# Kernel tuning notes

Measured on AMD Instinct MI355X. Metric: run time of the kernel, lower is better.

## Reference

```python
import jax, jax.numpy as jnp
import numpy as np

NEG_SLOPE = 0.2  # PyG GATConv default negative_slope


def gat_conv(x, src, dst, n_nodes, W, a_src, a_dst, b, concat):
    # x: [N, F_in], W: [F_in, H*C], a_src/a_dst: [H, C], b: [H*C] or [C]
    H, C = a_src.shape
    h = (x @ W).reshape(n_nodes, H, C)              # [N, H, C]
    e_s = jnp.sum(h * a_src, axis=-1)               # [N, H]
    e_d = jnp.sum(h * a_dst, axis=-1)               # [N, H]
    e = jax.nn.leaky_relu(e_s[src] + e_d[dst], NEG_SLOPE)  # [E, H]
    # segment softmax over incoming edges of each destination node
    m = jax.ops.segment_max(e, dst, num_segments=n_nodes)
    m = jnp.where(jnp.isfinite(m), m, 0.0)
    p = jnp.exp(e - m[dst])                         # [E, H]
    s = jax.ops.segment_sum(p, dst, num_segments=n_nodes)
    alpha = p / (s[dst] + 1e-16)                    # [E, H]
    out = jax.ops.segment_sum(h[src] * alpha[:, :, None], dst, num_segments=n_nodes)  # [N, H, C]
    out = out.reshape(n_nodes, H * C) if concat else out.mean(axis=1)
    return out + b


def setup_inputs() -> dict:
    key = jax.random.key(0)
    ks = jax.random.split(key, 20)
    N, E = 50000, 800000
    F_in, C, H = 128, 64, 4
    sc = 0.05
    inp = {
        "x": jax.random.normal(ks[0], (N, F_in), dtype=jnp.float32),
        "edge_index": jax.random.randint(ks[1], (2, E), 0, N, dtype=jnp.int64),
        # conv1: F_in -> C x H heads, concat
        "W1": jax.random.normal(ks[2], (F_in, H * C), dtype=jnp.float32) * sc,
        "a1_src": jax.random.normal(ks[3], (H, C), dtype=jnp.float32) * sc,
        "a1_dst": jax.random.normal(ks[4], (H, C), dtype=jnp.float32) * sc,
        "b1": jnp.zeros((H * C,), dtype=jnp.float32),
        # conv2: H*C -> C x H heads, concat
        "W2": jax.random.normal(ks[5], (H * C, H * C), dtype=jnp.float32) * sc,
        "a2_src": jax.random.normal(ks[6], (H, C), dtype=jnp.float32) * sc,
        "a2_dst": jax.random.normal(ks[7], (H, C), dtype=jnp.float32) * sc,
        "b2": jnp.zeros((H * C,), dtype=jnp.float32),
        # conv3: H*C -> C, 1 head, concat=False (mean)
        "W3": jax.random.normal(ks[8], (H * C, C), dtype=jnp.float32) * sc,
        "a3_src": jax.random.normal(ks[9], (1, C), dtype=jnp.float32) * sc,
        "a3_dst": jax.random.normal(ks[10], (1, C), dtype=jnp.float32) * sc,
        "b3": jnp.zeros((C,), dtype=jnp.float32),
        # node classification head: C -> 2
        "cls_W": jax.random.normal(ks[11], (C, 2), dtype=jnp.float32) * sc,
        "cls_b": jnp.zeros((2,), dtype=jnp.float32),
    }
    return inp


def reference(x, edge_index, W1, a1_src, a1_dst, b1, W2, a2_src, a2_dst, b2,
              W3, a3_src, a3_dst, b3, cls_W, cls_b):
    N = x.shape[0]
    # PyG GATConv default: add self loops
    loop = jnp.arange(N, dtype=edge_index.dtype)
    ei = jnp.concatenate([edge_index, jnp.stack([loop, loop])], axis=1)
    src, dst = ei[0], ei[1]

    h = jax.nn.elu(gat_conv(x, src, dst, N, W1, a1_src, a1_dst, b1, concat=True))
    h = jax.nn.elu(gat_conv(h, src, dst, N, W2, a2_src, a2_dst, b2, concat=True))
    h = gat_conv(h, src, dst, N, W3, a3_src, a3_dst, b3, concat=False)  # [N, C]

    node_output = h @ cls_W + cls_b  # [N, 2]
    link_embedding = h               # [N, C]
    return node_output, link_embedding
```

## Files before the change

### kernel.cpp

```cpp
#include <hip/hip_runtime.h>
#include <math.h>


typedef unsigned short ushort;
typedef __attribute__((ext_vector_type(8))) short bf16x8;
typedef __attribute__((ext_vector_type(4))) float f32x4;

#define LOG2E 1.4426950408889634f

static __device__ __forceinline__ ushort f2bf(float f) {
    unsigned x = __float_as_uint(f);
    unsigned r = (x + 0x7FFF + ((x >> 16) & 1)) >> 16;
    return (ushort)r;
}
static __device__ __forceinline__ float bf2f(ushort u) {
    return __uint_as_float(((unsigned)u) << 16);
}


__global__ void count_deg(const int* __restrict__ ei, int E, int* __restrict__ deg) {
    int i = blockIdx.x * blockDim.x + threadIdx.x;
    int stride = gridDim.x * blockDim.x;
    for (int e = i; e < E; e += stride) {
        int d = ei[E + e];
        atomicAdd(&deg[d], 1);
    }
}

__global__ void scan_local(const int* __restrict__ deg, int* __restrict__ offsets,
                           int* __restrict__ blockSums, int N) {
    int tid = threadIdx.x;
    int lane = tid & 63;
    int wv = tid >> 6;
    int base = blockIdx.x * 1024 + tid * 4;
    int v[4];
#pragma unroll
    for (int j = 0; j < 4; ++j) {
        int idx = base + j;
        v[j] = (idx < N) ? ((deg[idx] + 1 + 7) & ~7) : 0;
    }
    int tsum = v[0] + v[1] + v[2] + v[3];
    int inc = tsum;
#pragma unroll
    for (int off = 1; off < 64; off <<= 1) {
        int u = __shfl_up(inc, off);
        if (lane >= off) inc += u;
    }
    __shared__ int wtot[4];
    if (lane == 63) wtot[wv] = inc;
    __syncthreads();
    int wbase = 0;
#pragma unroll
    for (int w = 0; w < 4; ++w)
        if (w < wv) wbase += wtot[w];
    int run = wbase + inc - tsum;
#pragma unroll
    for (int j = 0; j < 4; ++j) {
        int idx = base + j;
        if (idx < N) offsets[idx] = run;
        run += v[j];
    }
    if (tid == 255) blockSums[blockIdx.x] = wbase + inc;
}

__global__ void scan_blocks(const int* __restrict__ blockSums, int* __restrict__ blockBase,
                            int* __restrict__ offsets, int N, int nblk) {
    int lane = threadIdx.x & 63;
    int v = (lane < nblk) ? blockSums[lane] : 0;
    int inc = v;
#pragma unroll
    for (int off = 1; off < 64; off <<= 1) {
        int u = __shfl_up(inc, off);
        if (lane >= off) inc += u;
    }
    if (lane < nblk) blockBase[lane] = inc - v;
    if (lane == 63) offsets[N] = inc;
}

__global__ void scan_add(int* __restrict__ offsets, const int* __restrict__ blockBase, int N) {
    int i = blockIdx.x * blockDim.x + threadIdx.x;
    if (i < N) offsets[i] += blockBase[i >> 10];
}

__global__ void fill_sent(int* __restrict__ csr_src, int cap, int N) {
    int i = blockIdx.x * blockDim.x + threadIdx.x;
    if (i < cap) csr_src[i] = N;
}

__global__ void fill_self(const int* __restrict__ offsets, int* __restrict__ counter,
                          int* __restrict__ csr_src, int N) {
    int i = blockIdx.x * blockDim.x + threadIdx.x;
    if (i < N) {
        csr_src[offsets[i]] = i;
        counter[i] = 1;
    }
}

__global__ void fill_edges(const int* __restrict__ ei, int E,
                           const int* __restrict__ offsets, int* __restrict__ counter,
                           int* __restrict__ csr_src) {
    int i = blockIdx.x * blockDim.x + threadIdx.x;
    int stride = gridDim.x * blockDim.x;
    for (int e = i; e < E; e += stride) {
        int s = ei[e];
        int d = ei[E + e];
        int pos = offsets[d] + atomicAdd(&counter[d], 1);
        csr_src[pos] = s;
    }
}


__global__ void xsplit(const float* __restrict__ X, ushort* __restrict__ Xh,
                       ushort* __restrict__ Xl, int total4) {
    int i = blockIdx.x * blockDim.x + threadIdx.x;
    if (i >= total4) return;
    float4 v = *(const float4*)(X + (size_t)i * 4);
    ushort4 h, l;
    h.x = f2bf(v.x); l.x = f2bf(v.x - bf2f(h.x));
    h.y = f2bf(v.y); l.y = f2bf(v.y - bf2f(h.y));
    h.z = f2bf(v.z); l.z = f2bf(v.z - bf2f(h.z));
    h.w = f2bf(v.w); l.w = f2bf(v.w - bf2f(h.w));
    *(ushort4*)(Xh + (size_t)i * 4) = h;
    *(ushort4*)(Xl + (size_t)i * 4) = l;
}

__global__ void wtrans_bf(const float* __restrict__ W, ushort* __restrict__ Wt,
                          int K, int N) {
    int id = blockIdx.x * blockDim.x + threadIdx.x;
    if (id >= K * N) return;
    int k = id % K, n = id / K;
    Wt[id] = f2bf(W[(size_t)k * N + n]);
}


template<int BM, int BN, int WM, int WN, int THREADS>
__global__ __launch_bounds__(THREADS) void gemm_mfma(const ushort* __restrict__ Ah,
                                                     const ushort* __restrict__ Al,
                                                     const ushort* __restrict__ Bh,
                                                     ushort* __restrict__ Cb,
                                                     int M, int N, int K) {
    constexpr int BK = 32, PAD = 8;
    constexpr int MI = BM / WM / 16;
    constexpr int NI = BN / WN / 16;
    static_assert(WM * WN * 64 == THREADS, "wave grid mismatch");
    __shared__ ushort As[2][BM][BK + PAD];
    __shared__ ushort Bs[BN][BK + PAD];

    int tid = threadIdx.x;
    int lane = tid & 63;
    int wid = tid >> 6;
    int fr = lane & 15;
    int fg = lane >> 4;
    int wm0 = (wid / WN) * (BM / WM);
    int wn0 = (wid % WN) * (BN / WN);
    int mBase = blockIdx.x * BM;
    int nBase = blockIdx.y * BN;

    f32x4 acc[MI][NI];
#pragma unroll
    for (int mi = 0; mi < MI; ++mi)
#pragma unroll
        for (int ni = 0; ni < NI; ++ni) acc[mi][ni] = (f32x4)0.0f;

    constexpr int ACH = BM * BK / 8;
    constexpr int BCH = BN * BK / 8;

    const int KI = K / BK;
    for (int t = 0; t < KI; ++t) {
        int k0 = t * BK;
        for (int q = tid; q < ACH; q += THREADS) {
            int row = q >> 2;
            int sl = (q & 3) * 8;
            int gm = mBase + row;
            if (gm >= M) gm = M - 1;
            size_t off = (size_t)gm * K + k0 + sl;
            *(bf16x8*)&As[0][row][sl] = *(const bf16x8*)(Ah + off);
            *(bf16x8*)&As[1][row][sl] = *(const bf16x8*)(Al + off);
        }
        for (int q = tid; q < BCH; q += THREADS) {
            int row = q >> 2;
            int sl = (q & 3) * 8;
            size_t off = (size_t)(nBase + row) * K + k0 + sl;
            *(bf16x8*)&Bs[row][sl] = *(const bf16x8*)(Bh + off);
        }
        __syncthreads();

        bf16x8 afh[MI], afl[MI], bfh[NI];
#pragma unroll
        for (int mi = 0; mi < MI; ++mi) {
            afh[mi] = *(const bf16x8*)&As[0][wm0 + mi * 16 + fr][fg * 8];
            afl[mi] = *(const bf16x8*)&As[1][wm0 + mi * 16 + fr][fg * 8];
        }
#pragma unroll
        for (int ni = 0; ni < NI; ++ni)
            bfh[ni] = *(const bf16x8*)&Bs[wn0 + ni * 16 + fr][fg * 8];
#pragma unroll
        for (int mi = 0; mi < MI; ++mi)
#pragma unroll
            for (int ni = 0; ni < NI; ++ni) {
                acc[mi][ni] = __builtin_amdgcn_mfma_f32_16x16x32_bf16(
                    afh[mi], bfh[ni], acc[mi][ni], 0, 0, 0);
                acc[mi][ni] = __builtin_amdgcn_mfma_f32_16x16x32_bf16(
                    afl[mi], bfh[ni], acc[mi][ni], 0, 0, 0);
            }
        __syncthreads();
    }

#pragma unroll
    for (int mi = 0; mi < MI; ++mi) {
#pragma unroll
        for (int j = 0; j < 4; ++j) {
            int gm = mBase + wm0 + mi * 16 + fg * 4 + j;
            if (gm >= M) continue;
#pragma unroll
            for (int ni = 0; ni < NI; ++ni) {
                int gn = nBase + wn0 + ni * 16 + fr;
                Cb[(size_t)gm * N + gn] = f2bf(acc[mi][ni][j]);
            }
        }
    }
}


template<int HC, int H>
__global__ void attn_coef(ushort* __restrict__ hb,
                          const float* __restrict__ a_src,
                          const float* __restrict__ a_dst,
                          float* __restrict__ e_s, float* __restrict__ e_d, int N) {
    int wid = (int)((blockIdx.x * (size_t)blockDim.x + threadIdx.x) >> 6);
    int lane = threadIdx.x & 63;
    if (wid > N) return;
    if (wid == N) {
        if constexpr (HC == 256) {
            ushort4 z = {0, 0, 0, 0};
            *(ushort4*)(hb + (size_t)N * 256 + lane * 4) = z;
        } else {
            hb[(size_t)N * HC + lane] = 0;
        }
        if (lane < H) e_s[(size_t)N * H + lane] = -1e30f;
        return;
    }
    if constexpr (HC == 256) {
        ushort4 q = *(const ushort4*)(hb + (size_t)wid * 256 + lane * 4);
        float4 as = *(const float4*)(a_src + lane * 4);
        float4 ad = *(const float4*)(a_dst + lane * 4);
        float h0 = bf2f(q.x), h1 = bf2f(q.y), h2 = bf2f(q.z), h3 = bf2f(q.w);
        float ps = h0 * as.x + h1 * as.y + h2 * as.z + h3 * as.w;
        float pd = h0 * ad.x + h1 * ad.y + h2 * ad.z + h3 * ad.w;
#pragma unroll
        for (int off = 1; off <= 8; off <<= 1) {
            ps += __shfl_xor(ps, off);
            pd += __shfl_xor(pd, off);
        }
        if ((lane & 15) == 0) {
            int hd = lane >> 4;
            e_s[(size_t)wid * H + hd] = ps * LOG2E;
            e_d[(size_t)wid * H + hd] = pd * LOG2E;
        }
    } else {
        float hv = bf2f(hb[(size_t)wid * HC + lane]);
        float ps = hv * a_src[lane];
        float pd = hv * a_dst[lane];
#pragma unroll
        for (int off = 1; off <= 32; off <<= 1) {
            ps += __shfl_xor(ps, off);
            pd += __shfl_xor(pd, off);
        }
        if (lane == 0) {
            e_s[wid] = ps * LOG2E;
            e_d[wid] = pd * LOG2E;
        }
    }
}


template<int HC, int H, bool ELU, bool SPLIT>
__global__ void aggregate(const ushort* __restrict__ hb,
                          const float* __restrict__ e_s, const float* __restrict__ e_d,
                          const int* __restrict__ offsets, const int* __restrict__ csr_src,
                          const float* __restrict__ bias,
                          float* __restrict__ out,
                          ushort* __restrict__ oh, ushort* __restrict__ ol, int N) {
    constexpr int U = 8;
    int wid = (int)((blockIdx.x * (size_t)blockDim.x + threadIdx.x) >> 6);
    int lane = threadIdx.x & 63;
    if (wid >= N) return;
    constexpr int VEC = HC / 64;
    constexpr int C = HC / H;
    constexpr int ROWSH = (HC == 256) ? 9 : 7;
    int hd = (lane * VEC) / C;
    float ed = e_d[(size_t)wid * H + hd];
    int beg = offsets[wid], end = offsets[wid + 1];
    const char* hbB = (const char*)hb;
    const char* esB = (const char*)e_s;
    unsigned laneOff = (unsigned)lane * (VEC * 2);

    float s = 0.0f;
    float acc[VEC];
#pragma unroll
    for (int j = 0; j < VEC; ++j) acc[j] = 0.0f;

    for (int k = beg; k < end; k += U) {
        int sidx[U];
#pragma unroll
        for (int u = 0; u < U; ++u) sidx[u] = csr_src[k + u];
        float e[U];
#pragma unroll
        for (int u = 0; u < U; ++u)
            e[u] = *(const float*)(esB + (((unsigned)(sidx[u] * H + hd)) << 2));
        ushort4 hv4[U];
        ushort  hv1[U];
        if constexpr (VEC == 4) {
#pragma unroll
            for (int u = 0; u < U; ++u)
                hv4[u] = *(const ushort4*)(hbB + (((unsigned)sidx[u]) << ROWSH) + laneOff);
        } else {
#pragma unroll
            for (int u = 0; u < U; ++u)
                hv1[u] = *(const ushort*)(hbB + (((unsigned)sidx[u]) << ROWSH) + laneOff);
        }
        float p[U];
        float psum = 0.0f;
#pragma unroll
        for (int u = 0; u < U; ++u) {
            float t = e[u] + ed;
            t = (t >= 0.0f) ? t : 0.2f * t;
            p[u] = __builtin_amdgcn_exp2f(t);
            psum += p[u];
        }
        s += psum;
        if constexpr (VEC == 4) {
#pragma unroll
            for (int u = 0; u < U; ++u) {
                acc[0] += p[u] * bf2f(hv4[u].x);
                acc[1] += p[u] * bf2f(hv4[u].y);
                acc[2] += p[u] * bf2f(hv4[u].z);
                acc[3] += p[u] * bf2f(hv4[u].w);
            }
        } else {
#pragma unroll
            for (int u = 0; u < U; ++u) acc[0] += p[u] * bf2f(hv1[u]);
        }
    }
    float inv = 1.0f / (s + 1e-16f);
    float o[VEC];
#pragma unroll
    for (int j = 0; j < VEC; ++j) {
        int f = lane * VEC + j;
        o[j] = acc[j] * inv + bias[f];
        if constexpr (ELU) o[j] = (o[j] > 0.0f) ? o[j] : expm1f(o[j]);
    }
    if constexpr (SPLIT) {
        if constexpr (VEC == 4) {
            ushort4 h4, l4;
            h4.x = f2bf(o[0]); l4.x = f2bf(o[0] - bf2f(h4.x));
            h4.y = f2bf(o[1]); l4.y = f2bf(o[1] - bf2f(h4.y));
            h4.z = f2bf(o[2]); l4.z = f2bf(o[2] - bf2f(h4.z));
            h4.w = f2bf(o[3]); l4.w = f2bf(o[3] - bf2f(h4.w));
            *(ushort4*)(oh + (size_t)wid * HC + lane * 4) = h4;
            *(ushort4*)(ol + (size_t)wid * HC + lane * 4) = l4;
        } else {
            ushort h1 = f2bf(o[0]);
            oh[(size_t)wid * HC + lane] = h1;
            ol[(size_t)wid * HC + lane] = f2bf(o[0] - bf2f(h1));
        }
    } else {
#pragma unroll
        for (int j = 0; j < VEC; ++j)
            out[(size_t)wid * HC + lane * VEC + j] = o[j];
    }
}


__global__ void cls_head(const float* __restrict__ h3, const float* __restrict__ W,
                         const float* __restrict__ b, float* __restrict__ out, int N) {
    int wid = (int)((blockIdx.x * (size_t)blockDim.x + threadIdx.x) >> 6);
    int lane = threadIdx.x & 63;
    if (wid >= N) return;
    float v = h3[(size_t)wid * 64 + lane];
    float p0 = v * W[lane * 2 + 0];
    float p1 = v * W[lane * 2 + 1];
#pragma unroll
    for (int off = 1; off <= 32; off <<= 1) {
        p0 += __shfl_xor(p0, off);
        p1 += __shfl_xor(p1, off);
    }
    if (lane == 0) {
        out[(size_t)wid * 2 + 0] = p0 + b[0];
        out[(size_t)wid * 2 + 1] = p1 + b[1];
    }
}


extern "C" void kernel_launch(void* const* d_in, const int* in_sizes, int n_in,
                              void* d_out, int out_size, void* d_ws, size_t ws_size,
                              hipStream_t stream) {
    const float* x      = (const float*)d_in[0];
    const int*   ei     = (const int*)d_in[1];
    const float* W1     = (const float*)d_in[2];
    const float* a1_src = (const float*)d_in[3];
    const float* a1_dst = (const float*)d_in[4];
    const float* b1     = (const float*)d_in[5];
    const float* W2     = (const float*)d_in[6];
    const float* a2_src = (const float*)d_in[7];
    const float* a2_dst = (const float*)d_in[8];
    const float* b2     = (const float*)d_in[9];
    const float* W3     = (const float*)d_in[10];
    const float* a3_src = (const float*)d_in[11];
    const float* a3_dst = (const float*)d_in[12];
    const float* b3     = (const float*)d_in[13];
    const float* cls_W  = (const float*)d_in[14];
    const float* cls_b  = (const float*)d_in[15];

    const int N = in_sizes[0] / 128;
    const int E = in_sizes[1] / 2;
    const int ETcap = E + 8 * N + 64;
    const int HC = 256;
    const int nScanBlk = (N + 1023) / 1024;

    char* w = (char*)d_ws;
    auto carve = [&](size_t bytes) {
        char* p = w;
        w += (bytes + 255) & ~(size_t)255;
        return p;
    };
    int*    deg     = (int*)   carve((size_t)N * 4);
    int*    counter = (int*)   carve((size_t)N * 4);
    int*    offsets = (int*)   carve((size_t)(N + 1) * 4);
    int*    csr_src = (int*)   carve((size_t)ETcap * 4);
    int*    blkSums = (int*)   carve((size_t)64 * 4);
    int*    blkBase = (int*)   carve((size_t)64 * 4);
    float*  e_s     = (float*) carve((size_t)(N + 1) * 4 * 4);
    float*  e_d     = (float*) carve((size_t)N * 4 * 4);
    ushort* hb      = (ushort*)carve((size_t)(N + 1) * HC * 2);
    ushort* Ahi     = (ushort*)carve((size_t)N * HC * 2);
    ushort* Alo     = (ushort*)carve((size_t)N * HC * 2);
    ushort* W1t     = (ushort*)carve((size_t)128 * 256 * 2);
    ushort* W2t     = (ushort*)carve((size_t)256 * 256 * 2);
    ushort* W3t     = (ushort*)carve((size_t)256 * 64 * 2);
    (void)ws_size;

    float* out_node = (float*)d_out;
    float* out_link = (float*)d_out + 2 * (size_t)N;

    hipMemsetAsync(deg, 0, (size_t)N * 4, stream);
    int eblocks = (E + 255) / 256;
    if (eblocks > 2048) eblocks = 2048;
    count_deg<<<eblocks, 256, 0, stream>>>(ei, E, deg);
    scan_local<<<nScanBlk, 256, 0, stream>>>(deg, offsets, blkSums, N);
    scan_blocks<<<1, 64, 0, stream>>>(blkSums, blkBase, offsets, N, nScanBlk);
    scan_add<<<(N + 255) / 256, 256, 0, stream>>>(offsets, blkBase, N);
    fill_sent<<<(ETcap + 255) / 256, 256, 0, stream>>>(csr_src, ETcap, N);
    fill_self<<<(N + 255) / 256, 256, 0, stream>>>(offsets, counter, csr_src, N);
    fill_edges<<<eblocks, 256, 0, stream>>>(ei, E, offsets, counter, csr_src);

    xsplit<<<(N * 128 / 4 + 255) / 256, 256, 0, stream>>>(x, Ahi, Alo, N * 128 / 4);
    wtrans_bf<<<(128 * 256 + 255) / 256, 256, 0, stream>>>(W1, W1t, 128, 256);
    wtrans_bf<<<(256 * 256 + 255) / 256, 256, 0, stream>>>(W2, W2t, 256, 256);
    wtrans_bf<<<(256 * 64 + 255) / 256, 256, 0, stream>>>(W3, W3t, 256, 64);

    dim3 g12((N + 63) / 64, 1);
    dim3 g3((N + 63) / 64, 1);
    int nodeBlocks  = (N + 3) / 4;
    int nodeBlocksP = (N + 1 + 3) / 4;

    gemm_mfma<64, 256, 2, 4, 512><<<g12, 512, 0, stream>>>(Ahi, Alo, W1t, hb, N, 256, 128);
    attn_coef<256, 4><<<nodeBlocksP, 256, 0, stream>>>(hb, a1_src, a1_dst, e_s, e_d, N);
    aggregate<256, 4, true, true><<<nodeBlocks, 256, 0, stream>>>(
        hb, e_s, e_d, offsets, csr_src, b1, nullptr, Ahi, Alo, N);
    gemm_mfma<64, 256, 2, 4, 512><<<g12, 512, 0, stream>>>(Ahi, Alo, W2t, hb, N, 256, 256);
    attn_coef<256, 4><<<nodeBlocksP, 256, 0, stream>>>(hb, a2_src, a2_dst, e_s, e_d, N);
    aggregate<256, 4, true, true><<<nodeBlocks, 256, 0, stream>>>(
        hb, e_s, e_d, offsets, csr_src, b2, nullptr, Ahi, Alo, N);
    gemm_mfma<64, 64, 4, 2, 512><<<g3, 512, 0, stream>>>(Ahi, Alo, W3t, hb, N, 64, 256);
    attn_coef<64, 1><<<nodeBlocksP, 256, 0, stream>>>(hb, a3_src, a3_dst, e_s, e_d, N);
    aggregate<64, 1, false, false><<<nodeBlocks, 256, 0, stream>>>(
        hb, e_s, e_d, offsets, csr_src, b3, out_link, nullptr, nullptr, N);
    cls_head<<<nodeBlocks, 256, 0, stream>>>(out_link, cls_W, cls_b, out_node, N);
}
```

Measured before the change: 372.9 us.

## Fuse attention coefficients into GEMM epilogue and classifier head into aggregation

Computes the per-node source/destination attention logits directly from the MFMA accumulators in the GEMM epilogue, using shuffles, plus a shared-memory cross-wave reduction for the single-head layer. This removes the separate attn_coef kernels and their re-read of the bf16 features. The classifier head is folded into the last aggregation kernel, which removes the cls_head launch and its re-read of the output. Sentinel row initialisation moves to a tiny init kernel, and the CSR index loads are vectorised into int4 reads. The cost is extra epilogue work and register pressure in the GEMM, and the layer-3 sentinel handling is split between init_sent and the GEMM epilogue.

```diff
diff --git a/kernel.cpp b/kernel.cpp
--- a/kernel.cpp
+++ b/kernel.cpp
@@ -132,12 +132,29 @@
     Wt[id] = f2bf(W[(size_t)k * N + n]);
 }
 
-
-template<int BM, int BN, int WM, int WN, int THREADS>
+__global__ void init_sent(ushort* __restrict__ hb, float* __restrict__ e_s4,
+                          float* __restrict__ e_s3, int N) {
+    int t = threadIdx.x;
+    if (t < 64) {
+        ushort4 z = {0, 0, 0, 0};
+        *(ushort4*)(hb + (size_t)N * 256 + t * 4) = z;
+    } else if (t < 68) {
+        e_s4[(size_t)N * 4 + (t - 64)] = -1e30f;
+    } else if (t == 68) {
+        e_s3[N] = -1e30f;
+    }
+}
+
+
+template<int BM, int BN, int WM, int WN, int THREADS, int H>
 __global__ __launch_bounds__(THREADS) void gemm_mfma(const ushort* __restrict__ Ah,
                                                      const ushort* __restrict__ Al,
                                                      const ushort* __restrict__ Bh,
                                                      ushort* __restrict__ Cb,
+                                                     float* __restrict__ e_s,
+                                                     float* __restrict__ e_d,
+                                                     const float* __restrict__ a_src,
+                                                     const float* __restrict__ a_dst,
                                                      int M, int N, int K) {
     constexpr int BK = 32, PAD = 8;
     constexpr int MI = BM / WM / 16;
@@ -219,69 +236,95 @@
             }
         }
     }
-}
-
-
-template<int HC, int H>
-__global__ void attn_coef(ushort* __restrict__ hb,
-                          const float* __restrict__ a_src,
-                          const float* __restrict__ a_dst,
-                          float* __restrict__ e_s, float* __restrict__ e_d, int N) {
-    int wid = (int)((blockIdx.x * (size_t)blockDim.x + threadIdx.x) >> 6);
-    int lane = threadIdx.x & 63;
-    if (wid > N) return;
-    if (wid == N) {
-        if constexpr (HC == 256) {
+
+    float asv[NI], adv[NI];
+#pragma unroll
+    for (int ni = 0; ni < NI; ++ni) {
+        int col = wn0 + ni * 16 + fr;
+        asv[ni] = a_src[col];
+        adv[ni] = a_dst[col];
+    }
+    if constexpr (WN == H) {
+        const int head = wn0 / (BN / H);
+#pragma unroll
+        for (int mi = 0; mi < MI; ++mi) {
+#pragma unroll
+            for (int j = 0; j < 4; ++j) {
+                float ps = 0.0f, pd = 0.0f;
+#pragma unroll
+                for (int ni = 0; ni < NI; ++ni) {
+                    ps += acc[mi][ni][j] * asv[ni];
+                    pd += acc[mi][ni][j] * adv[ni];
+                }
+#pragma unroll
+                for (int off = 1; off <= 8; off <<= 1) {
+                    ps += __shfl_xor(ps, off);
+                    pd += __shfl_xor(pd, off);
+                }
+                int gm = mBase + wm0 + mi * 16 + fg * 4 + j;
+                if (fr == 0 && gm < M) {
+                    e_s[(size_t)gm * H + head] = ps * LOG2E;
+                    e_d[(size_t)gm * H + head] = pd * LOG2E;
+                }
+            }
+        }
+    } else {
+        __shared__ float esb[WN][BM];
+        __shared__ float edb[WN][BM];
+        int wc = wid % WN;
+#pragma unroll
+        for (int mi = 0; mi < MI; ++mi) {
+#pragma unroll
+            for (int j = 0; j < 4; ++j) {
+                float ps = 0.0f, pd = 0.0f;
+#pragma unroll
+                for (int ni = 0; ni < NI; ++ni) {
+                    ps += acc[mi][ni][j] * asv[ni];
+                    pd += acc[mi][ni][j] * adv[ni];
+                }
+#pragma unroll
+                for (int off = 1; off <= 8; off <<= 1) {
+                    ps += __shfl_xor(ps, off);
+                    pd += __shfl_xor(pd, off);
+                }
+                if (fr == 0) {
+                    int lr = wm0 + mi * 16 + fg * 4 + j;
+                    esb[wc][lr] = ps;
+                    edb[wc][lr] = pd;
+                }
+            }
+        }
+        __syncthreads();
+        if (tid < BM) {
+            int gm = mBase + tid;
+            if (gm < M) {
+                float ps = 0.0f, pd = 0.0f;
+#pragma unroll
+                for (int wcc = 0; wcc < WN; ++wcc) {
+                    ps += esb[wcc][tid];
+                    pd += edb[wcc][tid];
+                }
+                e_s[gm] = ps * LOG2E;
+                e_d[gm] = pd * LOG2E;
+            }
+        }
+        if (blockIdx.x == 0 && tid < 16) {
             ushort4 z = {0, 0, 0, 0};
-            *(ushort4*)(hb + (size_t)N * 256 + lane * 4) = z;
-        } else {
-            hb[(size_t)N * HC + lane] = 0;
-        }
-        if (lane < H) e_s[(size_t)N * H + lane] = -1e30f;
-        return;
-    }
-    if constexpr (HC == 256) {
-        ushort4 q = *(const ushort4*)(hb + (size_t)wid * 256 + lane * 4);
-        float4 as = *(const float4*)(a_src + lane * 4);
-        float4 ad = *(const float4*)(a_dst + lane * 4);
-        float h0 = bf2f(q.x), h1 = bf2f(q.y), h2 = bf2f(q.z), h3 = bf2f(q.w);
-        float ps = h0 * as.x + h1 * as.y + h2 * as.z + h3 * as.w;
-        float pd = h0 * ad.x + h1 * ad.y + h2 * ad.z + h3 * ad.w;
-#pragma unroll
-        for (int off = 1; off <= 8; off <<= 1) {
-            ps += __shfl_xor(ps, off);
-            pd += __shfl_xor(pd, off);
-        }
-        if ((lane & 15) == 0) {
-            int hd = lane >> 4;
-            e_s[(size_t)wid * H + hd] = ps * LOG2E;
-            e_d[(size_t)wid * H + hd] = pd * LOG2E;
-        }
-    } else {
-        float hv = bf2f(hb[(size_t)wid * HC + lane]);
-        float ps = hv * a_src[lane];
-        float pd = hv * a_dst[lane];
-#pragma unroll
-        for (int off = 1; off <= 32; off <<= 1) {
-            ps += __shfl_xor(ps, off);
-            pd += __shfl_xor(pd, off);
-        }
-        if (lane == 0) {
-            e_s[wid] = ps * LOG2E;
-            e_d[wid] = pd * LOG2E;
-        }
-    }
-}
-
-
-template<int HC, int H, bool ELU, bool SPLIT>
+            *(ushort4*)(Cb + (size_t)M * N + tid * 4) = z;
+        }
+    }
+}
+
+
+template<int HC, int H, bool ELU, bool SPLIT, bool CLS>
 __global__ void aggregate(const ushort* __restrict__ hb,
                           const float* __restrict__ e_s, const float* __restrict__ e_d,
                           const int* __restrict__ offsets, const int* __restrict__ csr_src,
                           const float* __restrict__ bias,
                           float* __restrict__ out,
-                          ushort* __restrict__ oh, ushort* __restrict__ ol, int N) {
-    constexpr int U = 8;
+                          ushort* __restrict__ oh, ushort* __restrict__ ol,
+                          const float* __restrict__ clsW, const float* __restrict__ clsB,
+                          float* __restrict__ outN, int N) {
     int wid = (int)((blockIdx.x * (size_t)blockDim.x + threadIdx.x) >> 6);
     int lane = threadIdx.x & 63;
     if (wid >= N) return;
@@ -300,29 +343,29 @@
 #pragma unroll
     for (int j = 0; j < VEC; ++j) acc[j] = 0.0f;
 
-    for (int k = beg; k < end; k += U) {
-        int sidx[U];
-#pragma unroll
-        for (int u = 0; u < U; ++u) sidx[u] = csr_src[k + u];
-        float e[U];
-#pragma unroll
-        for (int u = 0; u < U; ++u)
+    for (int k = beg; k < end; k += 8) {
+        int4 c0 = *(const int4*)(csr_src + k);
+        int4 c1 = *(const int4*)(csr_src + k + 4);
+        int sidx[8] = {c0.x, c0.y, c0.z, c0.w, c1.x, c1.y, c1.z, c1.w};
+        float e[8];
+#pragma unroll
+        for (int u = 0; u < 8; ++u)
             e[u] = *(const float*)(esB + (((unsigned)(sidx[u] * H + hd)) << 2));
-        ushort4 hv4[U];
-        ushort  hv1[U];
+        ushort4 hv4[8];
+        ushort  hv1[8];
         if constexpr (VEC == 4) {
 #pragma unroll
-            for (int u = 0; u < U; ++u)
+            for (int u = 0; u < 8; ++u)
                 hv4[u] = *(const ushort4*)(hbB + (((unsigned)sidx[u]) << ROWSH) + laneOff);
         } else {
 #pragma unroll
-            for (int u = 0; u < U; ++u)
+            for (int u = 0; u < 8; ++u)
                 hv1[u] = *(const ushort*)(hbB + (((unsigned)sidx[u]) << ROWSH) + laneOff);
         }
-        float p[U];
+        float p[8];
         float psum = 0.0f;
 #pragma unroll
-        for (int u = 0; u < U; ++u) {
+        for (int u = 0; u < 8; ++u) {
             float t = e[u] + ed;
             t = (t >= 0.0f) ? t : 0.2f * t;
             p[u] = __builtin_amdgcn_exp2f(t);
@@ -331,7 +374,7 @@
         s += psum;
         if constexpr (VEC == 4) {
 #pragma unroll
-            for (int u = 0; u < U; ++u) {
+            for (int u = 0; u < 8; ++u) {
                 acc[0] += p[u] * bf2f(hv4[u].x);
                 acc[1] += p[u] * bf2f(hv4[u].y);
                 acc[2] += p[u] * bf2f(hv4[u].z);
@@ -339,7 +382,7 @@
             }
         } else {
 #pragma unroll
-            for (int u = 0; u < U; ++u) acc[0] += p[u] * bf2f(hv1[u]);
+            for (int u = 0; u < 8; ++u) acc[0] += p[u] * bf2f(hv1[u]);
         }
     }
     float inv = 1.0f / (s + 1e-16f);
@@ -369,25 +412,18 @@
         for (int j = 0; j < VEC; ++j)
             out[(size_t)wid * HC + lane * VEC + j] = o[j];
     }
-}
-
-
-__global__ void cls_head(const float* __restrict__ h3, const float* __restrict__ W,
-                         const float* __restrict__ b, float* __restrict__ out, int N) {
-    int wid = (int)((blockIdx.x * (size_t)blockDim.x + threadIdx.x) >> 6);
-    int lane = threadIdx.x & 63;
-    if (wid >= N) return;
-    float v = h3[(size_t)wid * 64 + lane];
-    float p0 = v * W[lane * 2 + 0];
-    float p1 = v * W[lane * 2 + 1];
-#pragma unroll
-    for (int off = 1; off <= 32; off <<= 1) {
-        p0 += __shfl_xor(p0, off);
-        p1 += __shfl_xor(p1, off);
-    }
-    if (lane == 0) {
-        out[(size_t)wid * 2 + 0] = p0 + b[0];
-        out[(size_t)wid * 2 + 1] = p1 + b[1];
+    if constexpr (CLS) {
+        float p0 = o[0] * clsW[lane * 2 + 0];
+        float p1 = o[0] * clsW[lane * 2 + 1];
+#pragma unroll
+        for (int off = 1; off <= 32; off <<= 1) {
+            p0 += __shfl_xor(p0, off);
+            p1 += __shfl_xor(p1, off);
+        }
+        if (lane == 0) {
+            outN[(size_t)wid * 2 + 0] = p0 + clsB[0];
+            outN[(size_t)wid * 2 + 1] = p1 + clsB[1];
+        }
     }
 }
 
@@ -432,6 +468,8 @@
     int*    blkBase = (int*)   carve((size_t)64 * 4);
     float*  e_s     = (float*) carve((size_t)(N + 1) * 4 * 4);
     float*  e_d     = (float*) carve((size_t)N * 4 * 4);
+    float*  e_s3    = (float*) carve((size_t)(N + 1) * 4);
+    float*  e_d3    = (float*) carve((size_t)N * 4);
     ushort* hb      = (ushort*)carve((size_t)(N + 1) * HC * 2);
     ushort* Ahi     = (ushort*)carve((size_t)N * HC * 2);
     ushort* Alo     = (ushort*)carve((size_t)N * HC * 2);
@@ -458,23 +496,25 @@
     wtrans_bf<<<(128 * 256 + 255) / 256, 256, 0, stream>>>(W1, W1t, 128, 256);
     wtrans_bf<<<(256 * 256 + 255) / 256, 256, 0, stream>>>(W2, W2t, 256, 256);
     wtrans_bf<<<(256 * 64 + 255) / 256, 256, 0, stream>>>(W3, W3t, 256, 64);
+    init_sent<<<1, 256, 0, stream>>>(hb, e_s, e_s3, N);
 
     dim3 g12((N + 63) / 64, 1);
     dim3 g3((N + 63) / 64, 1);
-    int nodeBlocks  = (N + 3) / 4;
-    int nodeBlocksP = (N + 1 + 3) / 4;
-
-    gemm_mfma<64, 256, 2, 4, 512><<<g12, 512, 0, stream>>>(Ahi, Alo, W1t, hb, N, 256, 128);
-    attn_coef<256, 4><<<nodeBlocksP, 256, 0, stream>>>(hb, a1_src, a1_dst, e_s, e_d, N);
-    aggregate<256, 4, true, true><<<nodeBlocks, 256, 0, stream>>>(
-        hb, e_s, e_d, offsets, csr_src, b1, nullptr, Ahi, Alo, N);
-    gemm_mfma<64, 256, 2, 4, 512><<<g12, 512, 0, stream>>>(Ahi, Alo, W2t, hb, N, 256, 256);
-    attn_coef<256, 4><<<nodeBlocksP, 256, 0, stream>>>(hb, a2_src, a2_dst, e_s, e_d, N);
-    aggregate<256, 4, true, true><<<nodeBlocks, 256, 0, stream>>>(
-        hb, e_s, e_d, offsets, csr_src, b2, nullptr, Ahi, Alo, N);
-    gemm_mfma<64, 64, 4, 2, 512><<<g3, 512, 0, stream>>>(Ahi, Alo, W3t, hb, N, 64, 256);
-    attn_coef<64, 1><<<nodeBlocksP, 256, 0, stream>>>(hb, a3_src, a3_dst, e_s, e_d, N);
-    aggregate<64, 1, false, false><<<nodeBlocks, 256, 0, stream>>>(
-        hb, e_s, e_d, offsets, csr_src, b3, out_link, nullptr, nullptr, N);
-    cls_head<<<nodeBlocks, 256, 0, stream>>>(out_link, cls_W, cls_b, out_node, N);
-}
+    int nodeBlocks = (N + 3) / 4;
+
+    gemm_mfma<64, 256, 2, 4, 512, 4><<<g12, 512, 0, stream>>>(
+        Ahi, Alo, W1t, hb, e_s, e_d, a1_src, a1_dst, N, 256, 128);
+    aggregate<256, 4, true, true, false><<<nodeBlocks, 256, 0, stream>>>(
+        hb, e_s, e_d, offsets, csr_src, b1, nullptr, Ahi, Alo,
+        nullptr, nullptr, nullptr, N);
+    gemm_mfma<64, 256, 2, 4, 512, 4><<<g12, 512, 0, stream>>>(
+        Ahi, Alo, W2t, hb, e_s, e_d, a2_src, a2_dst, N, 256, 256);
+    aggregate<256, 4, true, true, false><<<nodeBlocks, 256, 0, stream>>>(
+        hb, e_s, e_d, offsets, csr_src, b2, nullptr, Ahi, Alo,
+        nullptr, nullptr, nullptr, N);
+    gemm_mfma<64, 64, 4, 2, 512, 1><<<g3, 512, 0, stream>>>(
+        Ahi, Alo, W3t, hb, e_s3, e_d3, a3_src, a3_dst, N, 64, 256);
+    aggregate<64, 1, false, false, true><<<nodeBlocks, 256, 0, stream>>>(
+        hb, e_s3, e_d3, offsets, csr_src, b3, out_link, nullptr, nullptr,
+        cls_W, cls_b, out_node, N);
+}
```

Measured after the change: 356.1 us. 1.05x faster.
